# Performance work log

Hardware: AMD Instinct MI355X
Metric: run time of the kernel (lower is better)

## Reference

```python
import jax, jax.numpy as jnp
import numpy as np

T_EPS = 1e-07
NUM_CAPSULE = 10
DIM_CAPSULE = 64
ROUTINGS = 5


def squash(x, axis=-1):
    # NOTE: this repo's 'squash' is just norm-division (no s/(1+s) factor)
    s = jnp.sum(x * x, axis=axis, keepdims=True)
    return x / jnp.sqrt(s + T_EPS)


def setup_inputs() -> dict:
    key = jax.random.key(0)
    k1, k2 = jax.random.split(key)
    B, N, D = 128, 512, 300
    M = NUM_CAPSULE * DIM_CAPSULE  # 640
    x = jax.random.normal(k1, (B, N, D), dtype=jnp.float32)
    # xavier_normal for shape (1, D, M): std = sqrt(2/(fan_in+fan_out))
    std = float(np.sqrt(2.0 / (D + M)))
    W = jax.random.normal(k2, (1, D, M), dtype=jnp.float32) * std
    return {"x": x, "W": W}


def reference(x, W):
    B, N, D = x.shape
    # u_hat_vecs: [B, num_capsule(i), input_num_capsule(j), dim_capsule(k)]
    u = jnp.einsum('bnd,dm->bnm', x, W[0])
    u = u.reshape(B, N, NUM_CAPSULE, DIM_CAPSULE).transpose(0, 2, 1, 3)
    b = jnp.zeros((B, NUM_CAPSULE, N), dtype=x.dtype)
    outputs = None
    for i in range(ROUTINGS):
        # softmax over the num_capsule axis (axis=1 of b), matching the
        # permute(0,2,1) -> softmax(dim=2) -> permute back in torch
        c = jax.nn.softmax(b, axis=1)
        outputs = squash(jnp.einsum('bij,bijk->bik', c, u))  # [B, num, dim]
        if i < ROUTINGS - 1:
            b = jnp.einsum('bik,bijk->bij', outputs, u)
    return outputs
```

## Files before the change

### kernel.cpp

```cpp
#include <hip/hip_runtime.h>
#include <hip/hip_bf16.h>
#include <stdint.h>

#define BQ 128
#define NJ 512
#define DD 300
#define NC 10
#define DC 64
#define MM 640
#define KP 320
#define RT 5

typedef __attribute__((ext_vector_type(8))) short short8;
typedef __attribute__((ext_vector_type(4))) float f32x4;


__global__ void k_cast_x(const float* __restrict__ x, __hip_bfloat16* __restrict__ xb) {
    int g = blockIdx.x * 256 + threadIdx.x;
    int row = g / 40, cg2 = g - row * 40;
    const float* src = x + (size_t)row * DD + cg2 * 8;
    float4 a = make_float4(0.f, 0.f, 0.f, 0.f), b4 = a;
    if (cg2 < 37) { a = *(const float4*)src; b4 = *(const float4*)(src + 4); }
    else if (cg2 == 37) { a = *(const float4*)src; }
    union { ushort u[8]; uint4 v; } o;
    float f[8] = {a.x, a.y, a.z, a.w, b4.x, b4.y, b4.z, b4.w};
#pragma unroll
    for (int e = 0; e < 8; ++e) {
        __hip_bfloat16 hh = __float2bfloat16(f[e]);
        o.u[e] = *(ushort*)&hh;
    }
    *(uint4*)(xb + (size_t)row * KP + cg2 * 8) = o.v;
}

__global__ void k_cast_w(const float* __restrict__ w, __hip_bfloat16* __restrict__ wt) {
    int idx = blockIdx.x * 256 + threadIdx.x;
    int m = idx / KP, k = idx - m * KP;
    float v = (k < DD) ? w[(size_t)k * MM + m] : 0.f;
    wt[idx] = __float2bfloat16(v);
}

__global__ void k_zero(float4* __restrict__ p) {
    p[blockIdx.x * 256 + threadIdx.x] = make_float4(0.f, 0.f, 0.f, 0.f);
}


__global__ __launch_bounds__(256)
void k_gemm(const __hip_bfloat16* __restrict__ A,
            const __hip_bfloat16* __restrict__ Bt,
            __hip_bfloat16* __restrict__ C,
            float* __restrict__ su) {
    __shared__ __align__(16) __hip_bfloat16 As[128 * 64];
    __shared__ __align__(16) __hip_bfloat16 Bs[128 * 64];

    const int L  = blockIdx.x;
    const int n0 = ((L >> 3) % 5) * 128;
    const int m0 = ((L / 40) * 8 + (L & 7)) * 128;
    const int t  = threadIdx.x;
    const int w  = t >> 6, lane = t & 63;
    const int wrow = (w >> 1) * 64, wcol = (w & 1) * 64;
    const int quad = lane >> 4, r = lane & 15;

    f32x4 acc[4][4] = {};

    const int srow = t >> 3;
    const int sl   = (t & 7) ^ (srow & 7);
    const __hip_bfloat16* ag = A  + (size_t)(m0 + srow) * KP + sl * 8;
    const __hip_bfloat16* bg = Bt + (size_t)(n0 + srow) * KP + sl * 8;

    for (int kt = 0; kt < KP / 64; ++kt) {
        __syncthreads();
#pragma unroll
        for (int s = 0; s < 4; ++s) {
            __builtin_amdgcn_global_load_lds(
                (const __attribute__((address_space(1))) void*)(ag + (size_t)s * 32 * KP + kt * 64),
                (__attribute__((address_space(3))) void*)(&As[s * 2048 + t * 8]), 16, 0, 0);
            __builtin_amdgcn_global_load_lds(
                (const __attribute__((address_space(1))) void*)(bg + (size_t)s * 32 * KP + kt * 64),
                (__attribute__((address_space(3))) void*)(&Bs[s * 2048 + t * 8]), 16, 0, 0);
        }
        __syncthreads();

#pragma unroll
        for (int hh = 0; hh < 2; ++hh) {
            short8 af[4], bf[4];
#pragma unroll
            for (int mi = 0; mi < 4; ++mi) {
                int rho = wrow + mi * 16 + r;
                int p = (hh * 4 + quad) ^ (rho & 7);
                af[mi] = *(const short8*)&As[rho * 64 + p * 8];
            }
#pragma unroll
            for (int ni = 0; ni < 4; ++ni) {
                int rho = wcol + ni * 16 + r;
                int p = (hh * 4 + quad) ^ (rho & 7);
                bf[ni] = *(const short8*)&Bs[rho * 64 + p * 8];
            }
#pragma unroll
            for (int mi = 0; mi < 4; ++mi)
#pragma unroll
                for (int ni = 0; ni < 4; ++ni)
                    acc[mi][ni] = __builtin_amdgcn_mfma_f32_16x16x32_bf16(
                        af[mi], bf[ni], acc[mi][ni], 0, 0, 0);
        }
    }

#pragma unroll
    for (int mi = 0; mi < 4; ++mi)
#pragma unroll
        for (int ni = 0; ni < 4; ++ni) {
            int col = n0 + wcol + ni * 16 + r;
#pragma unroll
            for (int p = 0; p < 4; ++p) {
                int row = m0 + wrow + mi * 16 + quad * 4 + p;
                C[(size_t)row * MM + col] = __float2bfloat16(acc[mi][ni][p]);
            }
        }

    float cs[4];
#pragma unroll
    for (int ni = 0; ni < 4; ++ni) {
        float s = 0.f;
#pragma unroll
        for (int mi = 0; mi < 4; ++mi)
#pragma unroll
            for (int p = 0; p < 4; ++p) s += acc[mi][ni][p];
        s += __shfl_xor(s, 16, 64);
        s += __shfl_xor(s, 32, 64);
        cs[ni] = s;
    }
    if (quad == 0) {
        int bb = m0 >> 9;
#pragma unroll
        for (int ni = 0; ni < 4; ++ni)
            atomicAdd(&su[(size_t)bb * MM + n0 + wcol + ni * 16 + r], cs[ni]);
    }
}


__global__ __launch_bounds__(640)
void k_comb(const float* __restrict__ src, float* __restrict__ dst,
            int nsrc, float scale) {
    int b = blockIdx.x, t = threadIdx.x;
    float s = 0.f;
    for (int q = 0; q < nsrc; ++q) s += src[(size_t)(b * nsrc + q) * MM + t];
    s *= scale;
    float sq = s * s;
#pragma unroll
    for (int m = 32; m >= 1; m >>= 1) sq += __shfl_xor(sq, m, 64);
    dst[(size_t)b * MM + t] = s * rsqrtf(sq + 1e-7f);
}


__global__ __launch_bounds__(256, 5)
void k_pass(const __hip_bfloat16* __restrict__ u, const float* __restrict__ out,
            float* __restrict__ pnext) {
    __shared__ __align__(16) float pored[4 * 32 * 20];

    const int t   = threadIdx.x;
    const int blk = blockIdx.x;
    const int b   = blk >> 4, six = blk & 15;
    const int w   = t >> 6;
    const int jd  = t >> 5, kg = t & 31;

    const ushort* ubase = (const ushort*)u
        + (size_t)(b * NJ + six * 32 + jd) * MM + kg * 2;

    uint uv[10];
#pragma unroll
    for (int i = 0; i < 10; ++i) uv[i] = *(const uint*)(ubase + i * 64);

    float2 oo[10];
#pragma unroll
    for (int i = 0; i < 10; ++i) oo[i] = *(const float2*)(out + (size_t)b * MM + i * 64 + kg * 2);

    float po[20];
#pragma unroll
    for (int e = 0; e < 20; ++e) po[e] = 0.f;

    for (int tt = 0; tt < 4; ++tt) {
        uint nv[10];
        if (tt < 3) {
            const ushort* nrow = ubase + (size_t)(tt + 1) * 8 * MM;
#pragma unroll
            for (int i = 0; i < 10; ++i) nv[i] = *(const uint*)(nrow + i * 64);
        }

        float bl[10];
#pragma unroll
        for (int i = 0; i < 10; ++i) {
            float u0 = __uint_as_float(uv[i] << 16);
            float u1 = __uint_as_float(uv[i] & 0xffff0000u);
            bl[i] = u0 * oo[i].x + u1 * oo[i].y;
        }
#pragma unroll
        for (int m = 1; m <= 16; m <<= 1)
#pragma unroll
            for (int i = 0; i < 10; ++i) bl[i] += __shfl_xor(bl[i], m, 64);

        float mx = -1e30f;
#pragma unroll
        for (int i = 0; i < 10; ++i) mx = fmaxf(mx, bl[i]);
        float ssum = 0.f;
#pragma unroll
        for (int i = 0; i < 10; ++i) { bl[i] = __expf(bl[i] - mx); ssum += bl[i]; }
        float inv = 1.f / ssum;

#pragma unroll
        for (int i = 0; i < 10; ++i) {
            float cc = bl[i] * inv;
            float u0 = __uint_as_float(uv[i] << 16);
            float u1 = __uint_as_float(uv[i] & 0xffff0000u);
            po[i * 2 + 0] += cc * u0;
            po[i * 2 + 1] += cc * u1;
        }

        if (tt < 3) {
#pragma unroll
            for (int i = 0; i < 10; ++i) uv[i] = nv[i];
        }
    }

#pragma unroll
    for (int e = 0; e < 20; ++e) po[e] += __shfl_xor(po[e], 32, 64);
    if ((t & 63) < 32) {
#pragma unroll
        for (int e = 0; e < 20; ++e) pored[(w * 32 + kg) * 20 + e] = po[e];
    }
    __syncthreads();
    for (int m = t; m < MM; m += 256) {
        int i = m >> 6, k = m & 63, kg2 = k >> 1, kd = k & 1;
        float s = 0.f;
#pragma unroll
        for (int ww = 0; ww < 4; ++ww) s += pored[(ww * 32 + kg2) * 20 + i * 2 + kd];
        pnext[(size_t)blk * MM + m] = s;
    }
}


extern "C" void kernel_launch(void* const* d_in, const int* in_sizes, int n_in,
                              void* d_out, int out_size, void* d_ws, size_t ws_size,
                              hipStream_t stream) {
    const float* x = (const float*)d_in[0];
    const float* W = (const float*)d_in[1];
    float* out = (float*)d_out;

    char* ws = (char*)d_ws;
    size_t o = 0;
    __hip_bfloat16* xb = (__hip_bfloat16*)(ws + o); o += (size_t)BQ * NJ * KP * 2;
    __hip_bfloat16* wt = (__hip_bfloat16*)(ws + o); o += (size_t)MM * KP * 2;
    __hip_bfloat16* u  = (__hip_bfloat16*)(ws + o); o += (size_t)BQ * NJ * MM * 2;
    float* pb  = (float*)(ws + o); o += (size_t)2048 * MM * 4;
    float* ob  = (float*)(ws + o); o += (size_t)BQ * MM * 4;
    float* su  = (float*)(ws + o); o += (size_t)BQ * MM * 4;

    k_cast_x<<<(BQ * NJ * 40) / 256, 256, 0, stream>>>(x, xb);
    k_cast_w<<<(MM * KP) / 256, 256, 0, stream>>>(W, wt);
    k_zero<<<(BQ * MM) / (4 * 256), 256, 0, stream>>>((float4*)su);
    k_gemm<<<2560, 256, 0, stream>>>(xb, wt, u, su);

    k_comb<<<BQ, 640, 0, stream>>>(su, ob, 1, 0.1f);
    k_pass<<<2048, 256, 0, stream>>>(u, ob, pb);
    k_comb<<<BQ, 640, 0, stream>>>(pb, ob, 16, 1.f);
    k_pass<<<2048, 256, 0, stream>>>(u, ob, pb);
    k_comb<<<BQ, 640, 0, stream>>>(pb, ob, 16, 1.f);
    k_pass<<<2048, 256, 0, stream>>>(u, ob, pb);
    k_comb<<<BQ, 640, 0, stream>>>(pb, ob, 16, 1.f);
    k_pass<<<2048, 256, 0, stream>>>(u, ob, pb);
    k_comb<<<BQ, 640, 0, stream>>>(pb, out, 16, 1.f);
}
```

Baseline: 280.4 us.

## Avoid materializing u by routing through x with folded W projections

Drops the large x·W GEMM that materialized u (B×N×640 bf16). Each routing pass instead computes logits as x·(W·out) with MFMA, and accumulates c-weighted sums of x (via a transposed copy of x). The projection through W and the squash are applied per batch in a small k_out kernel. This removes most of the memory traffic and FLOPs of the GEMM and of the u reads. In exchange it uses split hi/lo bf16 products to keep precision, adds a transpose kernel, and has per-pass kernels do W matvecs.

```diff
diff --git a/kernel.cpp b/kernel.cpp
--- a/kernel.cpp
+++ b/kernel.cpp
@@ -13,6 +13,8 @@
 
 typedef __attribute__((ext_vector_type(8))) short short8;
 typedef __attribute__((ext_vector_type(4))) float f32x4;
+
+__device__ inline float bf2f(ushort u) { return __uint_as_float((uint)u << 16); }
 
 
 __global__ void k_cast_x(const float* __restrict__ x, __hip_bfloat16* __restrict__ xb) {
@@ -45,194 +47,209 @@
 
 
 __global__ __launch_bounds__(256)
-void k_gemm(const __hip_bfloat16* __restrict__ A,
-            const __hip_bfloat16* __restrict__ Bt,
-            __hip_bfloat16* __restrict__ C,
-            float* __restrict__ su) {
-    __shared__ __align__(16) __hip_bfloat16 As[128 * 64];
-    __shared__ __align__(16) __hip_bfloat16 Bs[128 * 64];
-
-    const int L  = blockIdx.x;
-    const int n0 = ((L >> 3) % 5) * 128;
-    const int m0 = ((L / 40) * 8 + (L & 7)) * 128;
-    const int t  = threadIdx.x;
-    const int w  = t >> 6, lane = t & 63;
-    const int wrow = (w >> 1) * 64, wcol = (w & 1) * 64;
+void k_xt(const __hip_bfloat16* __restrict__ xb, __hip_bfloat16* __restrict__ xt,
+          float* __restrict__ sx) {
+    __shared__ ushort lt[64][76];
+    int blk = blockIdx.x;
+    int b = blk / 40, rem = blk - b * 40, jt = rem / 5, dt = rem - (rem / 5) * 5;
+    int t = threadIdx.x;
+    int r = t >> 2, c = t & 3;
+#pragma unroll
+    for (int h = 0; h < 2; ++h) {
+        uint4 v = *(const uint4*)((const ushort*)xb +
+            (size_t)(b * 512 + jt * 64 + r) * KP + dt * 64 + (c + 4 * h) * 8);
+        *(uint2*)&lt[r][(c + 4 * h) * 8]     = make_uint2(v.x, v.y);
+        *(uint2*)&lt[r][(c + 4 * h) * 8 + 4] = make_uint2(v.z, v.w);
+    }
+    __syncthreads();
+    int dr = t >> 2;
+    float s = 0.f;
+#pragma unroll
+    for (int h = 0; h < 2; ++h) {
+        int jc = c + 4 * h;
+        union { ushort u[8]; uint4 v; } o;
+#pragma unroll
+        for (int e = 0; e < 8; ++e) o.u[e] = lt[jc * 8 + e][dr];
+        *(uint4*)((ushort*)xt + (size_t)(b * KP + dt * 64 + dr) * 512 + jt * 64 + jc * 8) = o.v;
+#pragma unroll
+        for (int e = 0; e < 8; ++e) s += bf2f(o.u[e]);
+    }
+    s += __shfl_xor(s, 1, 64);
+    s += __shfl_xor(s, 2, 64);
+    if (c == 0) atomicAdd(&sx[b * KP + dt * 64 + dr], s);
+}
+
+
+__global__ __launch_bounds__(256)
+void k_pass(const __hip_bfloat16* __restrict__ xb, const __hip_bfloat16* __restrict__ xt,
+            const __hip_bfloat16* __restrict__ wot, float* __restrict__ pcx) {
+    __shared__ __align__(16) float c_lds[16][68];
+
+    const int t = threadIdx.x, w = t >> 6, lane = t & 63;
     const int quad = lane >> 4, r = lane & 15;
-
-    f32x4 acc[4][4] = {};
-
-    const int srow = t >> 3;
-    const int sl   = (t & 7) ^ (srow & 7);
-    const __hip_bfloat16* ag = A  + (size_t)(m0 + srow) * KP + sl * 8;
-    const __hip_bfloat16* bg = Bt + (size_t)(n0 + srow) * KP + sl * 8;
-
-    for (int kt = 0; kt < KP / 64; ++kt) {
-        __syncthreads();
-#pragma unroll
-        for (int s = 0; s < 4; ++s) {
-            __builtin_amdgcn_global_load_lds(
-                (const __attribute__((address_space(1))) void*)(ag + (size_t)s * 32 * KP + kt * 64),
-                (__attribute__((address_space(3))) void*)(&As[s * 2048 + t * 8]), 16, 0, 0);
-            __builtin_amdgcn_global_load_lds(
-                (const __attribute__((address_space(1))) void*)(bg + (size_t)s * 32 * KP + kt * 64),
-                (__attribute__((address_space(3))) void*)(&Bs[s * 2048 + t * 8]), 16, 0, 0);
-        }
-        __syncthreads();
-
-#pragma unroll
-        for (int hh = 0; hh < 2; ++hh) {
-            short8 af[4], bf[4];
-#pragma unroll
-            for (int mi = 0; mi < 4; ++mi) {
-                int rho = wrow + mi * 16 + r;
-                int p = (hh * 4 + quad) ^ (rho & 7);
-                af[mi] = *(const short8*)&As[rho * 64 + p * 8];
+    const int blk = blockIdx.x, b = blk >> 3, jb = blk & 7;
+    const int j0 = jb * 64 + w * 16;
+
+    f32x4 acc = {0.f, 0.f, 0.f, 0.f};
+    const ushort* aph = (const ushort*)wot + ((size_t)(b * 2 + 0) * 16 + r) * KP + quad * 8;
+    const ushort* apl = aph + 16 * KP;
+    const ushort* bp  = (const ushort*)xb + (size_t)(b * 512 + j0 + r) * KP + quad * 8;
+#pragma unroll
+    for (int ks = 0; ks < 10; ++ks) {
+        short8 bf = *(const short8*)(bp  + ks * 32);
+        short8 ah = *(const short8*)(aph + ks * 32);
+        short8 al = *(const short8*)(apl + ks * 32);
+        acc = __builtin_amdgcn_mfma_f32_16x16x32_bf16(ah, bf, acc, 0, 0, 0);
+        acc = __builtin_amdgcn_mfma_f32_16x16x32_bf16(al, bf, acc, 0, 0, 0);
+    }
+
+    float mx;
+    if (quad < 2)       mx = fmaxf(fmaxf(acc[0], acc[1]), fmaxf(acc[2], acc[3]));
+    else if (quad == 2) mx = fmaxf(acc[0], acc[1]);
+    else                mx = -1e30f;
+    mx = fmaxf(mx, __shfl_xor(mx, 16, 64));
+    mx = fmaxf(mx, __shfl_xor(mx, 32, 64));
+    float e0 = (quad < 3) ? __expf(acc[0] - mx) : 0.f;
+    float e1 = (quad < 3) ? __expf(acc[1] - mx) : 0.f;
+    float e2 = (quad < 2) ? __expf(acc[2] - mx) : 0.f;
+    float e3 = (quad < 2) ? __expf(acc[3] - mx) : 0.f;
+    float ss = e0 + e1 + e2 + e3;
+    ss += __shfl_xor(ss, 16, 64);
+    ss += __shfl_xor(ss, 32, 64);
+    float inv = 1.f / ss;
+    int col = w * 16 + r;
+    if (quad < 2) {
+        c_lds[quad * 4 + 0][col] = e0 * inv;
+        c_lds[quad * 4 + 1][col] = e1 * inv;
+        c_lds[quad * 4 + 2][col] = e2 * inv;
+        c_lds[quad * 4 + 3][col] = e3 * inv;
+    } else if (quad == 2) {
+        c_lds[8][col] = e0 * inv;
+        c_lds[9][col] = e1 * inv;
+    }
+    __syncthreads();
+
+    short8 a2h[2], a2l[2];
+#pragma unroll
+    for (int ks = 0; ks < 2; ++ks) {
+        const float* cp = &c_lds[r][ks * 32 + quad * 8];
+        union { ushort u[8]; short8 v; } H, L;
+#pragma unroll
+        for (int e = 0; e < 8; ++e) {
+            float cf = cp[e];
+            __hip_bfloat16 hh = __float2bfloat16(cf);
+            float hf = __bfloat162float(hh);
+            __hip_bfloat16 ll = __float2bfloat16(cf - hf);
+            H.u[e] = *(ushort*)&hh;
+            L.u[e] = *(ushort*)&ll;
+        }
+        a2h[ks] = H.v; a2l[ks] = L.v;
+    }
+    f32x4 cacc[5] = {};
+#pragma unroll
+    for (int nt = 0; nt < 5; ++nt) {
+        const ushort* bb = (const ushort*)xt +
+            (size_t)(b * KP + (w * 5 + nt) * 16 + r) * 512 + jb * 64 + quad * 8;
+        short8 b20 = *(const short8*)(bb);
+        short8 b21 = *(const short8*)(bb + 32);
+        cacc[nt] = __builtin_amdgcn_mfma_f32_16x16x32_bf16(a2h[0], b20, cacc[nt], 0, 0, 0);
+        cacc[nt] = __builtin_amdgcn_mfma_f32_16x16x32_bf16(a2l[0], b20, cacc[nt], 0, 0, 0);
+        cacc[nt] = __builtin_amdgcn_mfma_f32_16x16x32_bf16(a2h[1], b21, cacc[nt], 0, 0, 0);
+        cacc[nt] = __builtin_amdgcn_mfma_f32_16x16x32_bf16(a2l[1], b21, cacc[nt], 0, 0, 0);
+    }
+    float* pout = pcx + (size_t)(b * 8 + jb) * 10 * KP;
+#pragma unroll
+    for (int nt = 0; nt < 5; ++nt) {
+        int d = (w * 5 + nt) * 16 + r;
+        if (quad < 2) {
+#pragma unroll
+            for (int p = 0; p < 4; ++p) pout[(quad * 4 + p) * KP + d] = cacc[nt][p];
+        } else if (quad == 2) {
+            pout[8 * KP + d] = cacc[nt][0];
+            pout[9 * KP + d] = cacc[nt][1];
+        }
+    }
+}
+
+
+template<int MODE>
+__global__ __launch_bounds__(640)
+void k_out(const float* __restrict__ src, const float* __restrict__ W,
+           const __hip_bfloat16* __restrict__ wt, __hip_bfloat16* __restrict__ wot,
+           float* __restrict__ dst) {
+    __shared__ __align__(16) float cx[10 * KP];
+    __shared__ __align__(16) float outl[MM];
+    const int b = blockIdx.x, t = threadIdx.x;
+
+    {
+        int dd = (t >= KP) ? t - KP : t;
+        int ih = (t >= KP) ? 1 : 0;
+        if (MODE == 0) {
+            float v = 0.1f * src[b * KP + dd];
+#pragma unroll
+            for (int kk = 0; kk < 5; ++kk) cx[(2 * kk + ih) * KP + dd] = v;
+        } else {
+            const float* pp = src + (size_t)b * 8 * 10 * KP;
+#pragma unroll
+            for (int kk = 0; kk < 5; ++kk) {
+                float s = 0.f;
+#pragma unroll
+                for (int jbk = 0; jbk < 8; ++jbk)
+                    s += pp[jbk * 10 * KP + (2 * kk + ih) * KP + dd];
+                cx[(2 * kk + ih) * KP + dd] = s;
             }
-#pragma unroll
-            for (int ni = 0; ni < 4; ++ni) {
-                int rho = wcol + ni * 16 + r;
-                int p = (hh * 4 + quad) ^ (rho & 7);
-                bf[ni] = *(const short8*)&Bs[rho * 64 + p * 8];
+        }
+    }
+    __syncthreads();
+
+    const int i = t >> 6;
+    const ushort* wrow = (const ushort*)wt + (size_t)t * KP;
+    float po = 0.f;
+#pragma unroll
+    for (int kk = 0; kk < 40; ++kk) {
+        union { uint4 q; ushort u[8]; } wv;
+        wv.q = *(const uint4*)(wrow + kk * 8);
+        const float* cr = cx + i * KP + kk * 8;
+#pragma unroll
+        for (int e = 0; e < 8; ++e) po += bf2f(wv.u[e]) * cr[e];
+    }
+    float sq = po * po;
+#pragma unroll
+    for (int m = 32; m >= 1; m >>= 1) sq += __shfl_xor(sq, m, 64);
+    float ov = po * rsqrtf(sq + 1e-7f);
+    if (MODE == 2) { dst[(size_t)b * MM + t] = ov; return; }
+    outl[t] = ov;
+    __syncthreads();
+
+    const int d0 = t >> 1, hW = t & 1;
+    float wo[5];
+    if (d0 < DD) {
+        const float4* wr = (const float4*)(W + (size_t)d0 * MM);
+#pragma unroll
+        for (int ii = 0; ii < 5; ++ii) {
+            int ic = hW * 5 + ii;
+            const float4* ol = (const float4*)(outl + ic * 64);
+            float s = 0.f;
+#pragma unroll
+            for (int kk = 0; kk < 16; ++kk) {
+                float4 a = wr[ic * 16 + kk];
+                float4 o = ol[kk];
+                s += a.x * o.x + a.y * o.y + a.z * o.z + a.w * o.w;
             }
-#pragma unroll
-            for (int mi = 0; mi < 4; ++mi)
-#pragma unroll
-                for (int ni = 0; ni < 4; ++ni)
-                    acc[mi][ni] = __builtin_amdgcn_mfma_f32_16x16x32_bf16(
-                        af[mi], bf[ni], acc[mi][ni], 0, 0, 0);
-        }
-    }
-
-#pragma unroll
-    for (int mi = 0; mi < 4; ++mi)
-#pragma unroll
-        for (int ni = 0; ni < 4; ++ni) {
-            int col = n0 + wcol + ni * 16 + r;
-#pragma unroll
-            for (int p = 0; p < 4; ++p) {
-                int row = m0 + wrow + mi * 16 + quad * 4 + p;
-                C[(size_t)row * MM + col] = __float2bfloat16(acc[mi][ni][p]);
-            }
-        }
-
-    float cs[4];
-#pragma unroll
-    for (int ni = 0; ni < 4; ++ni) {
-        float s = 0.f;
-#pragma unroll
-        for (int mi = 0; mi < 4; ++mi)
-#pragma unroll
-            for (int p = 0; p < 4; ++p) s += acc[mi][ni][p];
-        s += __shfl_xor(s, 16, 64);
-        s += __shfl_xor(s, 32, 64);
-        cs[ni] = s;
-    }
-    if (quad == 0) {
-        int bb = m0 >> 9;
-#pragma unroll
-        for (int ni = 0; ni < 4; ++ni)
-            atomicAdd(&su[(size_t)bb * MM + n0 + wcol + ni * 16 + r], cs[ni]);
-    }
-}
-
-
-__global__ __launch_bounds__(640)
-void k_comb(const float* __restrict__ src, float* __restrict__ dst,
-            int nsrc, float scale) {
-    int b = blockIdx.x, t = threadIdx.x;
-    float s = 0.f;
-    for (int q = 0; q < nsrc; ++q) s += src[(size_t)(b * nsrc + q) * MM + t];
-    s *= scale;
-    float sq = s * s;
-#pragma unroll
-    for (int m = 32; m >= 1; m >>= 1) sq += __shfl_xor(sq, m, 64);
-    dst[(size_t)b * MM + t] = s * rsqrtf(sq + 1e-7f);
-}
-
-
-__global__ __launch_bounds__(256, 5)
-void k_pass(const __hip_bfloat16* __restrict__ u, const float* __restrict__ out,
-            float* __restrict__ pnext) {
-    __shared__ __align__(16) float pored[4 * 32 * 20];
-
-    const int t   = threadIdx.x;
-    const int blk = blockIdx.x;
-    const int b   = blk >> 4, six = blk & 15;
-    const int w   = t >> 6;
-    const int jd  = t >> 5, kg = t & 31;
-
-    const ushort* ubase = (const ushort*)u
-        + (size_t)(b * NJ + six * 32 + jd) * MM + kg * 2;
-
-    uint uv[10];
-#pragma unroll
-    for (int i = 0; i < 10; ++i) uv[i] = *(const uint*)(ubase + i * 64);
-
-    float2 oo[10];
-#pragma unroll
-    for (int i = 0; i < 10; ++i) oo[i] = *(const float2*)(out + (size_t)b * MM + i * 64 + kg * 2);
-
-    float po[20];
-#pragma unroll
-    for (int e = 0; e < 20; ++e) po[e] = 0.f;
-
-    for (int tt = 0; tt < 4; ++tt) {
-        uint nv[10];
-        if (tt < 3) {
-            const ushort* nrow = ubase + (size_t)(tt + 1) * 8 * MM;
-#pragma unroll
-            for (int i = 0; i < 10; ++i) nv[i] = *(const uint*)(nrow + i * 64);
-        }
-
-        float bl[10];
-#pragma unroll
-        for (int i = 0; i < 10; ++i) {
-            float u0 = __uint_as_float(uv[i] << 16);
-            float u1 = __uint_as_float(uv[i] & 0xffff0000u);
-            bl[i] = u0 * oo[i].x + u1 * oo[i].y;
-        }
-#pragma unroll
-        for (int m = 1; m <= 16; m <<= 1)
-#pragma unroll
-            for (int i = 0; i < 10; ++i) bl[i] += __shfl_xor(bl[i], m, 64);
-
-        float mx = -1e30f;
-#pragma unroll
-        for (int i = 0; i < 10; ++i) mx = fmaxf(mx, bl[i]);
-        float ssum = 0.f;
-#pragma unroll
-        for (int i = 0; i < 10; ++i) { bl[i] = __expf(bl[i] - mx); ssum += bl[i]; }
-        float inv = 1.f / ssum;
-
-#pragma unroll
-        for (int i = 0; i < 10; ++i) {
-            float cc = bl[i] * inv;
-            float u0 = __uint_as_float(uv[i] << 16);
-            float u1 = __uint_as_float(uv[i] & 0xffff0000u);
-            po[i * 2 + 0] += cc * u0;
-            po[i * 2 + 1] += cc * u1;
-        }
-
-        if (tt < 3) {
-#pragma unroll
-            for (int i = 0; i < 10; ++i) uv[i] = nv[i];
-        }
-    }
-
-#pragma unroll
-    for (int e = 0; e < 20; ++e) po[e] += __shfl_xor(po[e], 32, 64);
-    if ((t & 63) < 32) {
-#pragma unroll
-        for (int e = 0; e < 20; ++e) pored[(w * 32 + kg) * 20 + e] = po[e];
-    }
-    __syncthreads();
-    for (int m = t; m < MM; m += 256) {
-        int i = m >> 6, k = m & 63, kg2 = k >> 1, kd = k & 1;
-        float s = 0.f;
-#pragma unroll
-        for (int ww = 0; ww < 4; ++ww) s += pored[(ww * 32 + kg2) * 20 + i * 2 + kd];
-        pnext[(size_t)blk * MM + m] = s;
+            wo[ii] = s;
+        }
+    } else {
+#pragma unroll
+        for (int ii = 0; ii < 5; ++ii) wo[ii] = 0.f;
+    }
+#pragma unroll
+    for (int ii = 0; ii < 5; ++ii) {
+        int ic = hW * 5 + ii;
+        __hip_bfloat16 hh = __float2bfloat16(wo[ii]);
+        float hf = __bfloat162float(hh);
+        __hip_bfloat16 ll = __float2bfloat16(wo[ii] - hf);
+        wot[((size_t)(b * 2 + 0) * 16 + ic) * KP + d0] = hh;
+        wot[((size_t)(b * 2 + 1) * 16 + ic) * KP + d0] = ll;
     }
 }
 
@@ -246,25 +263,25 @@
 
     char* ws = (char*)d_ws;
     size_t o = 0;
-    __hip_bfloat16* xb = (__hip_bfloat16*)(ws + o); o += (size_t)BQ * NJ * KP * 2;
-    __hip_bfloat16* wt = (__hip_bfloat16*)(ws + o); o += (size_t)MM * KP * 2;
-    __hip_bfloat16* u  = (__hip_bfloat16*)(ws + o); o += (size_t)BQ * NJ * MM * 2;
-    float* pb  = (float*)(ws + o); o += (size_t)2048 * MM * 4;
-    float* ob  = (float*)(ws + o); o += (size_t)BQ * MM * 4;
-    float* su  = (float*)(ws + o); o += (size_t)BQ * MM * 4;
+    __hip_bfloat16* xb  = (__hip_bfloat16*)(ws + o); o += (size_t)BQ * NJ * KP * 2;
+    __hip_bfloat16* xt  = (__hip_bfloat16*)(ws + o); o += (size_t)BQ * KP * NJ * 2;
+    __hip_bfloat16* wt  = (__hip_bfloat16*)(ws + o); o += (size_t)MM * KP * 2;
+    __hip_bfloat16* wot = (__hip_bfloat16*)(ws + o); o += (size_t)BQ * 2 * 16 * KP * 2;
+    float* pcx = (float*)(ws + o); o += (size_t)BQ * 8 * 10 * KP * 4;
+    float* sx  = (float*)(ws + o); o += (size_t)BQ * KP * 4;
 
     k_cast_x<<<(BQ * NJ * 40) / 256, 256, 0, stream>>>(x, xb);
     k_cast_w<<<(MM * KP) / 256, 256, 0, stream>>>(W, wt);
-    k_zero<<<(BQ * MM) / (4 * 256), 256, 0, stream>>>((float4*)su);
-    k_gemm<<<2560, 256, 0, stream>>>(xb, wt, u, su);
-
-    k_comb<<<BQ, 640, 0, stream>>>(su, ob, 1, 0.1f);
-    k_pass<<<2048, 256, 0, stream>>>(u, ob, pb);
-    k_comb<<<BQ, 640, 0, stream>>>(pb, ob, 16, 1.f);
-    k_pass<<<2048, 256, 0, stream>>>(u, ob, pb);
-    k_comb<<<BQ, 640, 0, stream>>>(pb, ob, 16, 1.f);
-    k_pass<<<2048, 256, 0, stream>>>(u, ob, pb);
-    k_comb<<<BQ, 640, 0, stream>>>(pb, ob, 16, 1.f);
-    k_pass<<<2048, 256, 0, stream>>>(u, ob, pb);
-    k_comb<<<BQ, 640, 0, stream>>>(pb, out, 16, 1.f);
-}
+    k_zero<<<(BQ * KP * 4) / (16 * 256), 256, 0, stream>>>((float4*)sx);
+    k_xt<<<BQ * 40, 256, 0, stream>>>(xb, xt, sx);
+
+    k_out<0><<<BQ, 640, 0, stream>>>(sx, W, wt, wot, nullptr);
+    k_pass<<<BQ * 8, 256, 0, stream>>>(xb, xt, wot, pcx);
+    k_out<1><<<BQ, 640, 0, stream>>>(pcx, W, wt, wot, nullptr);
+    k_pass<<<BQ * 8, 256, 0, stream>>>(xb, xt, wot, pcx);
+    k_out<1><<<BQ, 640, 0, stream>>>(pcx, W, wt, wot, nullptr);
+    k_pass<<<BQ * 8, 256, 0, stream>>>(xb, xt, wot, pcx);
+    k_out<1><<<BQ, 640, 0, stream>>>(pcx, W, wt, wot, nullptr);
+    k_pass<<<BQ * 8, 256, 0, stream>>>(xb, xt, wot, pcx);
+    k_out<2><<<BQ, 640, 0, stream>>>(pcx, W, wt, wot, out);
+}
```

Result: slower. 425.9 us (+51.9%).
